# Kernel tuning notes

Measured on AMD Instinct MI355X. Metric: run time of the kernel, lower is better.

Reference implementation:

```python
import jax, jax.numpy as jnp
import numpy as np

N_NODES = 65536   # entity nodes across batched docs
N_EDGES = 32768   # edges per etype
D_CTX = 768       # PTM hidden size ('n' feature)
D_REL = 97        # relation_num (out_feature)
CHUNK = 1024      # edge chunk for the per-edge bilinear


def setup_inputs() -> dict:
    key = jax.random.key(0)
    ks = jax.random.split(key, 10)
    n = jax.random.normal(ks[0], (N_NODES, D_CTX), jnp.float32)
    e_inter = jax.random.normal(ks[1], (N_EDGES, D_REL), jnp.float32)
    e_intra = jax.random.normal(ks[2], (N_EDGES, D_REL), jnp.float32)
    # nn.Bilinear(768, 97, 1, bias=False): weight [1, 768, 97]
    W_bl = jax.random.normal(ks[3], (1, D_CTX, D_REL), jnp.float32) * 0.02
    # nn.Bilinear(194, 194, 97): weight [97, 194, 194], bias [97]
    W_bl1 = jax.random.normal(ks[4], (D_REL, 2 * D_REL, 2 * D_REL), jnp.float32) * 0.02
    b_bl1 = jnp.zeros((D_REL,), jnp.float32)
    src_inter = jax.random.randint(ks[5], (N_EDGES,), 0, N_NODES, jnp.int32)
    dst_inter = jax.random.randint(ks[6], (N_EDGES,), 0, N_NODES, jnp.int32)
    src_intra = jax.random.randint(ks[7], (N_EDGES,), 0, N_NODES, jnp.int32)
    dst_intra = jax.random.randint(ks[8], (N_EDGES,), 0, N_NODES, jnp.int32)
    return {"n": n, "e_inter": e_inter, "e_intra": e_intra,
            "W_bl": W_bl, "W_bl1": W_bl1, "b_bl1": b_bl1,
            "src_inter": src_inter, "dst_inter": dst_inter,
            "src_intra": src_intra, "dst_intra": dst_intra}


def reference(n, e_inter, e_intra, W_bl, W_bl1, b_bl1,
              src_inter, dst_inter, src_intra, dst_intra):
    num_nodes = n.shape[0]
    # node_reduce: score = bilinear(n[dst], e) -> softmax over incoming edges
    # bl(src_n, e) = n[dst] @ W_bl[0] @ e  (precompute node projection once)
    proj = n @ W_bl[0]                                  # [N, D_REL]

    def node_reduce(e, dst):
        s = jnp.sum(proj[dst] * e, axis=-1)             # per-edge score [E]
        smax = jax.ops.segment_max(s, dst, num_segments=num_nodes)
        ex = jnp.exp(s - smax[dst])
        denom = jax.ops.segment_sum(ex, dst, num_segments=num_nodes)
        alpha = ex / denom[dst]                          # segment softmax
        # attention-weighted sum of mailbox messages -> [N, D_REL]
        return jax.ops.segment_sum(e * alpha[:, None], dst, num_segments=num_nodes)

    # multi_update_all(..., 'stack') over etypes ['inter','intra'] then flatten
    rel = jnp.concatenate([node_reduce(e_inter, dst_inter),
                           node_reduce(e_intra, dst_intra)], axis=-1)  # [N, 194]

    def edge_gate(e, src, dst):
        s_rel = rel[src]                                 # [E, 194]
        d_rel = rel[dst]                                 # [E, 194]
        d_in = s_rel.shape[1]

        def f(args):
            s, d = args                                  # [CHUNK, 194]
            return jnp.einsum('ei,kij,ej->ek', s, W_bl1, d, optimize=True) + b_bl1

        gate = jax.lax.map(f, (s_rel.reshape(-1, CHUNK, d_in),
                               d_rel.reshape(-1, CHUNK, d_in)))
        gate = gate.reshape(e.shape[0], -1)              # [E, D_REL]
        return e + jax.nn.sigmoid(gate) * e

    out_inter = edge_gate(e_inter, src_inter, dst_inter)
    out_intra = edge_gate(e_intra, src_intra, dst_intra)
    return jnp.stack([out_inter, out_intra])             # [2, E, D_REL]
```

## Files before the change

### kernel.cpp

```cpp
#include <hip/hip_runtime.h>
#include <hip/hip_bf16.h>
#include <stdint.h>


typedef __attribute__((ext_vector_type(8))) short short8;
typedef __attribute__((ext_vector_type(4))) float f32x4;
typedef _Float16 half8 __attribute__((ext_vector_type(8)));

#define NN 65536
#define NE1 32768
#define NEG 65536
#define DC 768
#define DR 97
#define DR2 194
#define RELSTR 200
#define KI 194
#define KS 7
#define NT 7
#define EPB 128
#define SSTR 200
#define DSTR 232
#define PSTR 72
#define NDESC_G 2176

#define OFF_REL   0ull
#define OFF_BPK   52428800ull
#define OFF_IDX   62164992ull
#define OFF_SMAX  62427136ull
#define OFF_DEN   62951424ull
#define OFF_META  63475712ull
#define OFF_DESC  63475968ull
#define OFF_WPK   63510784ull

static __device__ __forceinline__ unsigned fkey(float f) {
    unsigned b = __float_as_uint(f);
    return (b & 0x80000000u) ? ~b : (b | 0x80000000u);
}
static __device__ __forceinline__ float funkey(unsigned k) {
    return __uint_as_float((k & 0x80000000u) ? (k & 0x7fffffffu) : ~k);
}
static __device__ __forceinline__ unsigned pk2(_Float16 a, _Float16 b) {
    union { _Float16 h[2]; unsigned u; } x;
    x.h[0] = a; x.h[1] = b;
    return x.u;
}
static __device__ __forceinline__ int nstate(bool zi, bool zx) {
    return zi ? (zx ? 3 : 2) : (zx ? 1 : 0);
}
static __device__ __forceinline__ int nsplit_of(int b) {
    return (b == 0) ? 7 : ((b == 1 || b == 2) ? 4 : 2);
}
static __device__ __forceinline__ int kindbase_of(int b) {
    const int kb[9] = {0, 9, 15, 7, 13, 19, 7, 13, 19};
    return kb[b];
}

__global__ void build_bpk(const float* __restrict__ W, half8* __restrict__ Bpk) {
    int id = blockIdx.x * blockDim.x + threadIdx.x;
    const int total = KI * KS * NT * 64;
    if (id >= total) return;
    int l = id & 63;
    int g = id >> 6;
    int t = g % NT;
    int ks = (g / NT) % KS;
    int i = g / (NT * KS);
    int kk = t * 16 + (l & 15);
    int jb = ks * 32 + (l >> 4) * 8;
    half8 pk;
#pragma unroll
    for (int m = 0; m < 8; ++m) {
        int j = jb + m;
        float f = (kk < DR && j < DR2) ? W[(size_t)kk * (DR2 * DR2) + i * DR2 + j] : 0.f;
        pk[m] = (_Float16)f;
    }
    Bpk[id] = pk;
}

__global__ void build_wpk(const float* __restrict__ Wb, half8* __restrict__ Wpk) {
    int id = blockIdx.x * blockDim.x + threadIdx.x;
    const int total = 24 * NT * 64;
    if (id >= total) return;
    int l = id & 63;
    int g = id >> 6;
    int t = g % NT;
    int k2 = g / NT;
    int col = t * 16 + (l & 15);
    int j0 = k2 * 32 + (l >> 4) * 8;
    half8 pk;
#pragma unroll
    for (int m = 0; m < 8; ++m) {
        float f = (col < DR) ? Wb[(size_t)(j0 + m) * DR + col] : 0.f;
        pk[m] = (_Float16)f;
    }
    Wpk[id] = pk;
}

__launch_bounds__(512, 8)
__global__ void proj_mfma(const float* __restrict__ nmat, const half8* __restrict__ Wpk,
                          float* __restrict__ proj) {
    __shared__ __align__(16) _Float16 a_lds[128][PSTR];
    int tid = threadIdx.x;
    int r0 = blockIdx.x << 7;
    int w = tid >> 6, lane = tid & 63;
    int er = (w << 4) + (lane & 15);
    int lk = lane >> 4;

    f32x4 acc[NT];
#pragma unroll
    for (int t = 0; t < NT; ++t) acc[t] = (f32x4){0.f, 0.f, 0.f, 0.f};

    int srow = tid >> 2;
    int sc0 = (tid & 3) << 4;
    const float* nrow = nmat + (size_t)(r0 + srow) * DC + sc0;

    for (int k0 = 0; k0 < DC; k0 += 64) {
        __syncthreads();
        {
            const f32x4* p = (const f32x4*)(nrow + k0);
            _Float16* dst = &a_lds[srow][sc0];
#pragma unroll
            for (int q = 0; q < 4; ++q) {
                f32x4 v = p[q];
                *(unsigned*)&dst[q * 4]     = pk2((_Float16)v[0], (_Float16)v[1]);
                *(unsigned*)&dst[q * 4 + 2] = pk2((_Float16)v[2], (_Float16)v[3]);
            }
        }
        __syncthreads();
#pragma unroll
        for (int kk = 0; kk < 2; ++kk) {
            half8 af = *(const half8*)&a_lds[er][kk * 32 + lk * 8];
            const half8* bp = Wpk + (size_t)((k0 >> 5) + kk) * (NT * 64) + lane;
#pragma unroll
            for (int t = 0; t < NT; ++t)
                acc[t] = __builtin_amdgcn_mfma_f32_16x16x32_f16(af, bp[t * 64], acc[t], 0, 0, 0);
        }
    }

#pragma unroll
    for (int t = 0; t < NT; ++t) {
        int col = t * 16 + (lane & 15);
        if (col < DR) {
#pragma unroll
            for (int r = 0; r < 4; ++r) {
                int row = r0 + (w << 4) + lk * 4 + r;
                proj[(size_t)row * DR + col] = acc[t][r];
            }
        }
    }
}

__global__ void score_kernel(const float* __restrict__ proj,
                             const float* __restrict__ e_inter, const float* __restrict__ e_intra,
                             const int* __restrict__ dst_inter, const int* __restrict__ dst_intra,
                             float* __restrict__ s_buf, unsigned* __restrict__ smax_key) {
    int wid = (blockIdx.x * blockDim.x + threadIdx.x) >> 6;
    int lane = threadIdx.x & 63;
    if (wid >= NEG) return;
    int et = wid >> 15, le = wid & (NE1 - 1);
    const float* e = (et ? e_intra : e_inter) + (size_t)le * DR;
    int dst = (et ? dst_intra : dst_inter)[le];
    const float* pr = proj + (size_t)dst * DR;
    float p = pr[lane] * e[lane];
    if (lane < DR - 64) p += pr[lane + 64] * e[lane + 64];
#pragma unroll
    for (int off = 32; off > 0; off >>= 1) p += __shfl_down(p, off);
    if (lane == 0) {
        s_buf[wid] = p;
        atomicMax(&smax_key[et * NN + dst], fkey(p));
    }
}

__global__ void accum_kernel(const float* __restrict__ s_buf,
                             const float* __restrict__ e_inter, const float* __restrict__ e_intra,
                             const int* __restrict__ dst_inter, const int* __restrict__ dst_intra,
                             const unsigned* __restrict__ smax_key,
                             float* __restrict__ denom, float* __restrict__ rel) {
    int wid = (blockIdx.x * blockDim.x + threadIdx.x) >> 6;
    int lane = threadIdx.x & 63;
    if (wid >= NEG) return;
    int et = wid >> 15, le = wid & (NE1 - 1);
    const float* e = (et ? e_intra : e_inter) + (size_t)le * DR;
    int dst = (et ? dst_intra : dst_inter)[le];
    float s = s_buf[wid];
    float mx = funkey(smax_key[et * NN + dst]);
    float ex = __expf(s - mx);
    if (lane == 0) atomicAdd(&denom[et * NN + dst], ex);
    float* rrow = rel + (size_t)dst * RELSTR + et * DR;
    atomicAdd(&rrow[lane], e[lane] * ex);
    if (lane < DR - 64) atomicAdd(&rrow[lane + 64], e[lane + 64] * ex);
}

__global__ void dinv_kernel(float* __restrict__ denom) {
    int i = blockIdx.x * blockDim.x + threadIdx.x;
    if (i < 2 * NN) {
        float d = denom[i];
        denom[i] = (d > 0.f) ? (1.f / d) : 0.f;
    }
}

__global__ void classify_kernel(const float* __restrict__ dinv,
                                const int* __restrict__ src_inter, const int* __restrict__ dst_inter,
                                const int* __restrict__ src_intra, const int* __restrict__ dst_intra,
                                unsigned* __restrict__ meta) {
    __shared__ unsigned h[16];
    if (threadIdx.x < 16) h[threadIdx.x] = 0;
    __syncthreads();
    int gid = blockIdx.x * blockDim.x + threadIdx.x;
    if (gid < NEG) {
        int et = gid >> 15, le = gid & (NE1 - 1);
        int sn = (et ? src_intra : src_inter)[le];
        int dn = (et ? dst_intra : dst_inter)[le];
        int ss = nstate(dinv[sn] == 0.f, dinv[NN + sn] == 0.f);
        int ds = nstate(dinv[dn] == 0.f, dinv[NN + dn] == 0.f);
        int b = (ss == 3 || ds == 3) ? 9 : ss * 3 + ds;
        atomicAdd(&h[b], 1u);
    }
    __syncthreads();
    if (threadIdx.x < 10 && h[threadIdx.x])
        atomicAdd(&meta[threadIdx.x], h[threadIdx.x]);
}

__global__ void setup1_kernel(unsigned* __restrict__ meta) {
    if (threadIdx.x != 0 || blockIdx.x != 0) return;
    unsigned run = 0;
    for (int b = 0; b < 10; ++b) {
        meta[32 + b] = run;
        meta[16 + b] = run;
        run += meta[b];
    }
    unsigned c = 0;
    for (int b = 0; b < 9; ++b) {
        meta[52 + b] = c;
        c += ((meta[b] + EPB - 1) / EPB) * (unsigned)nsplit_of(b);
    }
    meta[48] = c;
}

__global__ void setup2_kernel(const unsigned* __restrict__ meta, uint4* __restrict__ desc) {
    int j = blockIdx.x * blockDim.x + threadIdx.x;
    if (j >= (int)meta[48]) return;
    int b = 8;
    for (int q = 1; q < 9; ++q)
        if (j < (int)meta[52 + q]) { b = q - 1; break; }
    int p = j - (int)meta[52 + b];
    int ns = nsplit_of(b);
    int ci = p / ns;
    int si = p - ci * ns;
    int cnt = (int)meta[b];
    int cbase = (int)meta[32 + b] + ci * EPB;
    int ccnt = cnt - ci * EPB;
    if (ccnt > EPB) ccnt = EPB;
    int kind = kindbase_of(b) + si;
    int sclass = b / 3;
    desc[j] = make_uint4((unsigned)kind, (unsigned)cbase, (unsigned)ccnt, (unsigned)sclass);
}

__global__ void scatter_kernel(const float* __restrict__ dinv,
                               const int* __restrict__ src_inter, const int* __restrict__ dst_inter,
                               const int* __restrict__ src_intra, const int* __restrict__ dst_intra,
                               unsigned* __restrict__ meta, int* __restrict__ idxbuf) {
    __shared__ unsigned cur[16];
    __shared__ unsigned base[16];
    if (threadIdx.x < 16) cur[threadIdx.x] = 0;
    __syncthreads();
    int gid = blockIdx.x * blockDim.x + threadIdx.x;
    int b = -1;
    unsigned r = 0;
    if (gid < NEG) {
        int et = gid >> 15, le = gid & (NE1 - 1);
        int sn = (et ? src_intra : src_inter)[le];
        int dn = (et ? dst_intra : dst_inter)[le];
        int ss = nstate(dinv[sn] == 0.f, dinv[NN + sn] == 0.f);
        int ds = nstate(dinv[dn] == 0.f, dinv[NN + dn] == 0.f);
        b = (ss == 3 || ds == 3) ? 9 : ss * 3 + ds;
        r = atomicAdd(&cur[b], 1u);
    }
    __syncthreads();
    if (threadIdx.x < 10 && cur[threadIdx.x])
        base[threadIdx.x] = atomicAdd(&meta[16 + threadIdx.x], cur[threadIdx.x]);
    __syncthreads();
    if (b >= 0) idxbuf[base[b] + r] = gid;
}

__global__ void skip_kernel(const unsigned* __restrict__ meta, const int* __restrict__ idxbuf,
                            const float* __restrict__ e_inter, const float* __restrict__ e_intra,
                            const float* __restrict__ bias, float* __restrict__ out) {
    int n9 = (int)meta[9];
    int base9 = (int)meta[41];
    int k = threadIdx.x;
    float g = 0.f;
    if (k < DR) {
        float b = bias[k];
        g = 1.f + 1.f / (1.f + __expf(-b));
    }
    for (int q = blockIdx.x; q < n9; q += gridDim.x) {
        int gid = idxbuf[base9 + q];
        int et = gid >> 15, le = gid & (NE1 - 1);
        const float* e = (et ? e_intra : e_inter) + (size_t)le * DR;
        if (k < DR) out[(size_t)gid * DR + k] = e[k] * g;
    }
}

template <int KS0, int KS1, int T0, int T1>
static __device__ __forceinline__ void gate_piece(
    const _Float16 (*__restrict__ s_lds)[SSTR],
    const _Float16 (*__restrict__ d_lds)[DSTR],
    const half8* __restrict__ Bpk, const float* __restrict__ bias,
    const float* __restrict__ e_inter, const float* __restrict__ e_intra,
    const int* __restrict__ idxbuf,
    int i0, int iEnd, int cbase, int ccnt, int w, int lane,
    float* __restrict__ out)
{
    constexpr int NKS = KS1 - KS0;
    constexpr int NTT = T1 - T0;
    int lk = lane >> 4;
    int er = (w << 4) + (lane & 15);

    half8 dv[NKS];
#pragma unroll
    for (int ks = 0; ks < NKS; ++ks)
        dv[ks] = *(const half8*)&d_lds[er][(KS0 + ks) * 32 + lk * 8];

    f32x4 acc[NTT];
#pragma unroll
    for (int tt = 0; tt < NTT; ++tt) acc[tt] = (f32x4){0.f, 0.f, 0.f, 0.f};

    const half8* bl = Bpk + lane;
    for (int i = i0; i < iEnd; ++i) {
        _Float16 sa = s_lds[er][i];
        half8 sv = {sa, sa, sa, sa, sa, sa, sa, sa};
        const half8* bi = bl + (size_t)((i * KS + KS0) * NT + T0) * 64;
#pragma unroll
        for (int ks = 0; ks < NKS; ++ks) {
            half8 af = sv * dv[ks];
#pragma unroll
            for (int tt = 0; tt < NTT; ++tt) {
                half8 bv = bi[(ks * NT + tt) * 64];
                acc[tt] = __builtin_amdgcn_mfma_f32_16x16x32_f16(af, bv, acc[tt], 0, 0, 0);
            }
        }
    }

#pragma unroll
    for (int r = 0; r < 4; ++r) {
        int row = (w << 4) + lk * 4 + r;
        if (row < ccnt) {
            int gid = idxbuf[cbase + row];
            int et = gid >> 15, le = gid & (NE1 - 1);
            const float* e = (et ? e_intra : e_inter) + (size_t)le * DR;
            float* o = out + (size_t)gid * DR;
#pragma unroll
            for (int tt = 0; tt < NTT; ++tt) {
                int k = (T0 + tt) * 16 + (lane & 15);
                if (k < DR) {
                    float g = acc[tt][r] + bias[k];
                    float sg = 1.f / (1.f + __expf(-g));
                    o[k] = e[k] * (1.f + sg);
                }
            }
        }
    }
}

__launch_bounds__(512, 1)
__global__ void gate_all(const float* __restrict__ rel, const float* __restrict__ dinv,
                         const half8* __restrict__ Bpk, const float* __restrict__ bias,
                         const int* __restrict__ src_inter, const int* __restrict__ dst_inter,
                         const int* __restrict__ src_intra, const int* __restrict__ dst_intra,
                         const float* __restrict__ e_inter, const float* __restrict__ e_intra,
                         const int* __restrict__ idxbuf, const unsigned* __restrict__ meta,
                         const uint4* __restrict__ desc, float* __restrict__ out) {
    if (blockIdx.x >= meta[48]) return;
    uint4 de = desc[blockIdx.x];
    int kind = (int)de.x;
    int cbase = (int)de.y;
    int ccnt = (int)de.z;
    int sclass = (int)de.w;
    int i0 = (sclass == 2) ? DR : 0;
    int iEnd = (sclass == 0) ? DR2 : (i0 + DR);

    __shared__ __align__(16) _Float16 s_lds[EPB][SSTR];
    __shared__ __align__(16) _Float16 d_lds[EPB][DSTR];
    int tid = threadIdx.x;

    {
        int r = tid >> 1;
        int h = tid & 1;
        int edge = r & 127;
        bool isd = (r >= 128);
        int rc = cbase + ((edge < ccnt) ? edge : (ccnt - 1));
        int gid = idxbuf[rc];
        int et = gid >> 15, le = gid & (NE1 - 1);
        int node = isd ? (et ? dst_intra : dst_inter)[le]
                       : (et ? src_intra : src_inter)[le];
        float di0 = dinv[node];
        float di1 = dinv[NN + node];
        const f32x4* rp = (const f32x4*)(rel + (size_t)node * RELSTR + h * 100);
        _Float16* row = isd ? &d_lds[edge][0] : &s_lds[edge][0];
#pragma unroll
        for (int q = 0; q < 25; ++q) {
            f32x4 v = rp[q];
            int c = h * 100 + q * 4;
            _Float16 h0 = (_Float16)(v[0] * ((c + 0 < DR) ? di0 : di1));
            _Float16 h1 = (_Float16)(v[1] * ((c + 1 < DR) ? di0 : di1));
            _Float16 h2 = (_Float16)(v[2] * ((c + 2 < DR) ? di0 : di1));
            _Float16 h3 = (_Float16)(v[3] * ((c + 3 < DR) ? di0 : di1));
            *(unsigned*)&row[c] = pk2(h0, h1);
            *(unsigned*)&row[c + 2] = pk2(h2, h3);
        }
        if (isd && h) {
            short8 z = (short8)(short)0;
#pragma unroll
            for (int q = 0; q < 3; ++q)
                *(short8*)&row[200 + q * 8] = z;
        }
    }
    __syncthreads();

    int w = tid >> 6;
    int lane = tid & 63;

#define GP(A, B, C, D) gate_piece<A, B, C, D>(s_lds, d_lds, Bpk, bias, e_inter, e_intra, \
                                              idxbuf, i0, iEnd, cbase, ccnt, w, lane, out)
    switch (kind) {
        case 0:  GP(0, 7, 0, 1); break;
        case 1:  GP(0, 7, 1, 2); break;
        case 2:  GP(0, 7, 2, 3); break;
        case 3:  GP(0, 7, 3, 4); break;
        case 4:  GP(0, 7, 4, 5); break;
        case 5:  GP(0, 7, 5, 6); break;
        case 6:  GP(0, 7, 6, 7); break;
        case 7:  GP(0, 7, 0, 4); break;
        case 8:  GP(0, 7, 4, 7); break;
        case 9:  GP(0, 4, 0, 2); break;
        case 10: GP(0, 4, 2, 4); break;
        case 11: GP(0, 4, 4, 6); break;
        case 12: GP(0, 4, 6, 7); break;
        case 13: GP(0, 4, 0, 4); break;
        case 14: GP(0, 4, 4, 7); break;
        case 15: GP(3, 7, 0, 2); break;
        case 16: GP(3, 7, 2, 4); break;
        case 17: GP(3, 7, 4, 6); break;
        case 18: GP(3, 7, 6, 7); break;
        case 19: GP(3, 7, 0, 4); break;
        case 20: GP(3, 7, 4, 7); break;
        default: break;
    }
#undef GP
}

extern "C" void kernel_launch(void* const* d_in, const int* in_sizes, int n_in,
                              void* d_out, int out_size, void* d_ws, size_t ws_size,
                              hipStream_t stream) {
    (void)in_sizes; (void)n_in; (void)out_size; (void)ws_size;
    const float* nmat     = (const float*)d_in[0];
    const float* e_inter  = (const float*)d_in[1];
    const float* e_intra  = (const float*)d_in[2];
    const float* W_bl     = (const float*)d_in[3];
    const float* W_bl1    = (const float*)d_in[4];
    const float* b_bl1    = (const float*)d_in[5];
    const int* src_inter  = (const int*)d_in[6];
    const int* dst_inter  = (const int*)d_in[7];
    const int* src_intra  = (const int*)d_in[8];
    const int* dst_intra  = (const int*)d_in[9];
    float* out = (float*)d_out;

    char* ws = (char*)d_ws;
    float* regA     = (float*)(ws + OFF_REL);
    half8* Bpk      = (half8*)(ws + OFF_BPK);
    int* idxbuf     = (int*)(ws + OFF_IDX);
    float* s_buf    = (float*)(ws + OFF_IDX);
    unsigned* smax  = (unsigned*)(ws + OFF_SMAX);
    float* denom    = (float*)(ws + OFF_DEN);
    unsigned* meta  = (unsigned*)(ws + OFF_META);
    uint4* desc     = (uint4*)(ws + OFF_DESC);
    half8* Wpk      = (half8*)(ws + OFF_WPK);

    hipMemsetAsync(smax, 0, 524288, stream);
    hipMemsetAsync(denom, 0, 524288, stream);
    hipMemsetAsync(meta, 0, 256, stream);

    build_bpk<<<(KI * KS * NT * 64 + 255) / 256, 256, 0, stream>>>(W_bl1, Bpk);
    build_wpk<<<(24 * NT * 64 + 255) / 256, 256, 0, stream>>>(W_bl, Wpk);
    proj_mfma<<<NN / 128, 512, 0, stream>>>(nmat, Wpk, regA);
    score_kernel<<<NEG / 4, 256, 0, stream>>>(regA, e_inter, e_intra, dst_inter, dst_intra,
                                              s_buf, smax);
    hipMemsetAsync(regA, 0, 52428800, stream);
    accum_kernel<<<NEG / 4, 256, 0, stream>>>(s_buf, e_inter, e_intra, dst_inter, dst_intra,
                                              smax, denom, regA);
    dinv_kernel<<<512, 256, 0, stream>>>(denom);
    classify_kernel<<<NEG / 256, 256, 0, stream>>>(denom, src_inter, dst_inter,
                                                   src_intra, dst_intra, meta);
    setup1_kernel<<<1, 64, 0, stream>>>(meta);
    setup2_kernel<<<(NDESC_G + 255) / 256, 256, 0, stream>>>(meta, desc);
    scatter_kernel<<<NEG / 256, 256, 0, stream>>>(denom, src_inter, dst_inter,
                                                  src_intra, dst_intra, meta, idxbuf);
    skip_kernel<<<2048, 128, 0, stream>>>(meta, idxbuf, e_inter, e_intra, b_bl1, out);
    gate_all<<<NDESC_G, 512, 0, stream>>>(regA, denom, Bpk, b_bl1,
                                          src_inter, dst_inter, src_intra, dst_intra,
                                          e_inter, e_intra, idxbuf, meta, desc, out);
}
```

Measured before the change: 662.4 us.

## Load dst rel fragments straight to registers, drop d_lds, raise occupancy

Removes the shared-memory staging buffer for destination relation rows. Each lane now gathers its own d fragments from global rel, scales them by dinv and converts them to half in registers. This cuts LDS use per block roughly in half and raises launch_bounds min-blocks from 1 to 4, so more blocks can be resident to hide latency. In exchange it adds redundant global gathers across lanes and tighter register limits that may cause spills.

Result: slower. 1.020 ms (+53.9%).

```diff
diff --git a/kernel.cpp b/kernel.cpp
--- a/kernel.cpp
+++ b/kernel.cpp
@@ -19,7 +19,6 @@
 #define NT 7
 #define EPB 128
 #define SSTR 200
-#define DSTR 232
 #define PSTR 72
 #define NDESC_G 2176
 
@@ -304,7 +303,8 @@
 template <int KS0, int KS1, int T0, int T1>
 static __device__ __forceinline__ void gate_piece(
     const _Float16 (*__restrict__ s_lds)[SSTR],
-    const _Float16 (*__restrict__ d_lds)[DSTR],
+    const float* __restrict__ rel, const float* __restrict__ dinv,
+    const int* __restrict__ dst_inter, const int* __restrict__ dst_intra,
     const half8* __restrict__ Bpk, const float* __restrict__ bias,
     const float* __restrict__ e_inter, const float* __restrict__ e_intra,
     const int* __restrict__ idxbuf,
@@ -317,9 +317,32 @@
     int er = (w << 4) + (lane & 15);
 
     half8 dv[NKS];
-#pragma unroll
-    for (int ks = 0; ks < NKS; ++ks)
-        dv[ks] = *(const half8*)&d_lds[er][(KS0 + ks) * 32 + lk * 8];
+    {
+        int rc = cbase + ((er < ccnt) ? er : (ccnt - 1));
+        int gid = idxbuf[rc];
+        int et = gid >> 15, le = gid & (NE1 - 1);
+        int dn = (et ? dst_intra : dst_inter)[le];
+        float di0 = dinv[dn], di1 = dinv[NN + dn];
+        const float* drow = rel + (size_t)dn * RELSTR;
+#pragma unroll
+        for (int ks = 0; ks < NKS; ++ks) {
+            constexpr int KSA_BASE = KS0;
+            int ksa = KSA_BASE + ks;
+            int j0 = ksa * 32 + lk * 8;
+            half8 hh = {0, 0, 0, 0, 0, 0, 0, 0};
+            if (!(ksa == 6 && lk > 0)) {
+                const f32x4* p = (const f32x4*)(drow + j0);
+                f32x4 v0 = p[0], v1 = p[1];
+#pragma unroll
+                for (int m = 0; m < 4; ++m)
+                    hh[m] = (_Float16)(v0[m] * ((j0 + m < DR) ? di0 : di1));
+#pragma unroll
+                for (int m = 0; m < 4; ++m)
+                    hh[4 + m] = (_Float16)(v1[m] * ((j0 + 4 + m < DR) ? di0 : di1));
+            }
+            dv[ks] = hh;
+        }
+    }
 
     f32x4 acc[NTT];
 #pragma unroll
@@ -362,7 +385,7 @@
     }
 }
 
-__launch_bounds__(512, 1)
+__launch_bounds__(512, 4)
 __global__ void gate_all(const float* __restrict__ rel, const float* __restrict__ dinv,
                          const half8* __restrict__ Bpk, const float* __restrict__ bias,
                          const int* __restrict__ src_inter, const int* __restrict__ dst_inter,
@@ -380,23 +403,19 @@
     int iEnd = (sclass == 0) ? DR2 : (i0 + DR);
 
     __shared__ __align__(16) _Float16 s_lds[EPB][SSTR];
-    __shared__ __align__(16) _Float16 d_lds[EPB][DSTR];
     int tid = threadIdx.x;
 
-    {
-        int r = tid >> 1;
+    if (tid < 256) {
+        int edge = tid >> 1;
         int h = tid & 1;
-        int edge = r & 127;
-        bool isd = (r >= 128);
         int rc = cbase + ((edge < ccnt) ? edge : (ccnt - 1));
         int gid = idxbuf[rc];
         int et = gid >> 15, le = gid & (NE1 - 1);
-        int node = isd ? (et ? dst_intra : dst_inter)[le]
-                       : (et ? src_intra : src_inter)[le];
-        float di0 = dinv[node];
-        float di1 = dinv[NN + node];
-        const f32x4* rp = (const f32x4*)(rel + (size_t)node * RELSTR + h * 100);
-        _Float16* row = isd ? &d_lds[edge][0] : &s_lds[edge][0];
+        int sn = (et ? src_intra : src_inter)[le];
+        float di0 = dinv[sn];
+        float di1 = dinv[NN + sn];
+        const f32x4* rp = (const f32x4*)(rel + (size_t)sn * RELSTR + h * 100);
+        _Float16* row = &s_lds[edge][0];
 #pragma unroll
         for (int q = 0; q < 25; ++q) {
             f32x4 v = rp[q];
@@ -408,20 +427,15 @@
             *(unsigned*)&row[c] = pk2(h0, h1);
             *(unsigned*)&row[c + 2] = pk2(h2, h3);
         }
-        if (isd && h) {
-            short8 z = (short8)(short)0;
-#pragma unroll
-            for (int q = 0; q < 3; ++q)
-                *(short8*)&row[200 + q * 8] = z;
-        }
     }
     __syncthreads();
 
     int w = tid >> 6;
     int lane = tid & 63;
 
-#define GP(A, B, C, D) gate_piece<A, B, C, D>(s_lds, d_lds, Bpk, bias, e_inter, e_intra, \
-                                              idxbuf, i0, iEnd, cbase, ccnt, w, lane, out)
+#define GP(A, B, C, D) gate_piece<A, B, C, D>(s_lds, rel, dinv, dst_inter, dst_intra, \
+                                              Bpk, bias, e_inter, e_intra, idxbuf,    \
+                                              i0, iEnd, cbase, ccnt, w, lane, out)
     switch (kind) {
         case 0:  GP(0, 7, 0, 1); break;
         case 1:  GP(0, 7, 1, 2); break;
```
